# Kernel tuning notes

Hardware: AMD Instinct MI355X
Metric: run time of the kernel (lower is better)

Reference implementation:

```python
import jax, jax.numpy as jnp
import numpy as np

B, N = 8, 16384
DIMS = [3, 64, 128, 1024]  # conv1d(kernel=1) channel sizes: in -> layer_dims -> feat_size
EPS = 1e-5  # BatchNorm1d default eps


def setup_inputs() -> dict:
    key = jax.random.key(0)
    ks = jax.random.split(key, 8)
    inp = {"x": jax.random.normal(ks[0], (B, N, 3), dtype=jnp.float32)}
    for i in range(3):
        cin, cout = DIMS[i], DIMS[i + 1]
        k1, k2 = jax.random.split(ks[i + 1])
        inp[f"W{i}"] = jax.random.normal(k1, (cout, cin), dtype=jnp.float32) * (1.0 / np.sqrt(cin))
        inp[f"b{i}"] = jax.random.normal(k2, (cout,), dtype=jnp.float32) * 0.01
        inp[f"g{i}"] = jnp.ones((cout,), dtype=jnp.float32)   # BN gamma (init 1)
        inp[f"be{i}"] = jnp.zeros((cout,), dtype=jnp.float32)  # BN beta (init 0)
    return inp


def _bn(h, gamma, beta):
    # training-mode BatchNorm1d: stats over batch and point dims, biased variance
    m = h.mean(axis=(0, 1))
    v = h.var(axis=(0, 1))
    return (h - m) * jax.lax.rsqrt(v + EPS) * gamma + beta


def reference(x, W0, b0, g0, be0, W1, b1, g1, be1, W2, b2, g2, be2):
    # pointwise Conv1d (kernel=1) == per-point linear; layout (B, N, C)
    h = jax.nn.relu(_bn(jnp.einsum('bnc,oc->bno', x, W0) + b0, g0, be0))
    local = h  # (B, N, 64) local features
    h = jax.nn.relu(_bn(jnp.einsum('bnc,oc->bno', h, W1) + b1, g1, be1))
    h = _bn(jnp.einsum('bnc,oc->bno', h, W2) + b2, g2, be2)  # no relu on last layer
    gfeat = h.max(axis=1)  # (B, 1024) global max-pool over points
    # concat broadcast global feature with local features -> (B, 1024+64, N) in torch layout
    out = jnp.concatenate(
        [jnp.broadcast_to(gfeat[:, :, None], (B, DIMS[-1], N)), jnp.swapaxes(local, 1, 2)], axis=1)
    return out
```

## Files before the change

### kernel.cpp

```cpp
#include <hip/hip_runtime.h>


#define P_TOT  131072
#define NPTS   16384
#define EPSF   1e-5f

typedef __bf16 bf16x8 __attribute__((ext_vector_type(8)));
typedef float  f32x4  __attribute__((ext_vector_type(4)));

#define H0_OFF   0u
#define H1_OFF   16777216u
#define W1B_OFF  50331648u
#define W2B_OFF  50348032u
#define ST_OFF   50610176u
#define MM_OFF   50662400u

#define S0   0
#define Q0   64
#define S1   128
#define Q1   256
#define S2   384
#define Q2   1408
#define SC0  2432
#define SH0  2496
#define SC1  2560
#define SH1  2688
#define GF   4864
#define STATS_ZERO_N 2432

__device__ __forceinline__ unsigned short f2bf(float f) {
  unsigned u = __builtin_bit_cast(unsigned, f);
  u += 0x7fffu + ((u >> 16) & 1u);
  return (unsigned short)(u >> 16);
}
__device__ __forceinline__ float bf2f(unsigned short s) {
  return __builtin_bit_cast(float, ((unsigned)s) << 16);
}
__device__ __forceinline__ unsigned encf(float f) {
  unsigned u = __builtin_bit_cast(unsigned, f);
  return (u & 0x80000000u) ? ~u : (u | 0x80000000u);
}
__device__ __forceinline__ float decf(unsigned e) {
  unsigned u = (e & 0x80000000u) ? (e & 0x7fffffffu) : ~e;
  return __builtin_bit_cast(float, u);
}
__device__ __forceinline__ uint4 pack8(const float* f) {
  uint4 r;
  r.x = (unsigned)f2bf(f[0]) | ((unsigned)f2bf(f[1]) << 16);
  r.y = (unsigned)f2bf(f[2]) | ((unsigned)f2bf(f[3]) << 16);
  r.z = (unsigned)f2bf(f[4]) | ((unsigned)f2bf(f[5]) << 16);
  r.w = (unsigned)f2bf(f[6]) | ((unsigned)f2bf(f[7]) << 16);
  return r;
}
__device__ __forceinline__ uint4 bnrelu8(uint4 v, const float* sc, const float* sh) {
  unsigned vv[4] = {v.x, v.y, v.z, v.w};
  float f[8];
#pragma unroll
  for (int i = 0; i < 4; ++i) {
    float a = bf2f((unsigned short)(vv[i] & 0xffffu));
    float b = bf2f((unsigned short)(vv[i] >> 16));
    f[2*i]   = fmaxf(fmaf(a, sc[2*i],   sh[2*i]),   0.f);
    f[2*i+1] = fmaxf(fmaf(b, sc[2*i+1], sh[2*i+1]), 0.f);
  }
  return pack8(f);
}

__global__ __launch_bounds__(256) void k_init(const float* __restrict__ W1,
                                              const float* __restrict__ W2,
                                              unsigned short* __restrict__ w1b,
                                              unsigned short* __restrict__ w2b,
                                              float* __restrict__ stats,
                                              unsigned* __restrict__ mmx) {
  int tid = blockIdx.x * 256 + threadIdx.x;
  int stride = gridDim.x * 256;
  for (int i = tid; i < 1024 * 128; i += stride) w2b[i] = f2bf(W2[i]);
  for (int i = tid; i < 128 * 64;   i += stride) w1b[i] = f2bf(W1[i]);
  for (int i = tid; i < STATS_ZERO_N; i += stride) stats[i] = 0.f;
  for (int i = tid; i < 8192; i += stride) { mmx[i] = 0u; mmx[8192 + i] = 0xffffffffu; }
}

__global__ __launch_bounds__(256) void k_layer0(const float* __restrict__ x,
                                                const float* __restrict__ W0,
                                                unsigned short* __restrict__ h0b,
                                                float* __restrict__ stats) {
  __shared__ float w0s[192];
  __shared__ float bs[64], bq[64];
  int t = threadIdx.x;
  if (t < 192) w0s[t] = W0[t];
  if (t < 64) { bs[t] = 0.f; bq[t] = 0.f; }
  __syncthreads();
  int p  = blockIdx.x * 64 + (t >> 2);
  int cs = (t & 3) * 16;
  float x0 = x[p*3], x1 = x[p*3+1], x2 = x[p*3+2];
  float v[16];
#pragma unroll
  for (int j = 0; j < 16; ++j) {
    int c = cs + j;
    v[j] = x0 * w0s[c*3] + x1 * w0s[c*3+1] + x2 * w0s[c*3+2];
  }
  uint4* dst = (uint4*)(h0b + p*64 + cs);
  dst[0] = pack8(&v[0]);
  dst[1] = pack8(&v[8]);
  int lane = t & 63;
#pragma unroll
  for (int j = 0; j < 16; ++j) {
    float s = v[j], q = v[j]*v[j];
#pragma unroll
    for (int m = 4; m < 64; m <<= 1) { s += __shfl_xor(s, m, 64); q += __shfl_xor(q, m, 64); }
    if (lane < 4) { atomicAdd(&bs[cs + j], s); atomicAdd(&bq[cs + j], q); }
  }
  __syncthreads();
  if (t < 64) { atomicAdd(&stats[S0 + t], bs[t]); atomicAdd(&stats[Q0 + t], bq[t]); }
}

__global__ void k_fin0(const float* __restrict__ g, const float* __restrict__ be,
                       float* __restrict__ stats) {
  int c = threadIdx.x;
  float m = stats[S0 + c] * (1.f / P_TOT);
  float q = stats[Q0 + c] * (1.f / P_TOT);
  float sc = g[c] * rsqrtf(q - m*m + EPSF);
  stats[SC0 + c] = sc;
  stats[SH0 + c] = be[c] - m * sc;
}
__global__ void k_fin1(const float* __restrict__ g, const float* __restrict__ be,
                       float* __restrict__ stats) {
  int c = threadIdx.x;
  float m = stats[S1 + c] * (1.f / P_TOT);
  float q = stats[Q1 + c] * (1.f / P_TOT);
  float sc = g[c] * rsqrtf(q - m*m + EPSF);
  stats[SC1 + c] = sc;
  stats[SH1 + c] = be[c] - m * sc;
}

__global__ __launch_bounds__(512, 2) void k_gemm1(const unsigned short* __restrict__ h0b,
                                                  const unsigned short* __restrict__ w1b,
                                                  unsigned short* __restrict__ h1b,
                                                  float* __restrict__ stats) {
  __shared__ uint4 arrA[128 * 8];
  int t = threadIdx.x, l = t & 63, w = t >> 6;
  int wr = w >> 2, wc = w & 3;
  bf16x8 bfr[2][2];
#pragma unroll
  for (int nn = 0; nn < 2; ++nn)
#pragma unroll
    for (int kk = 0; kk < 2; ++kk) {
      int j  = wc*32 + nn*16 + (l & 15);
      int k0 = kk*32 + (l >> 4) * 8;
      bfr[nn][kk] = __builtin_bit_cast(bf16x8, *(const uint4*)(w1b + j*64 + k0));
    }
  int kc = t & 7;
  float ssc[8], ssh[8];
#pragma unroll
  for (int j = 0; j < 8; ++j) { ssc[j] = stats[SC0 + kc*8 + j]; ssh[j] = stats[SH0 + kc*8 + j]; }
  float runS[2] = {0,0}, runQ[2] = {0,0};
  int pbase0 = blockIdx.x * 256;
  for (int mt = 0; mt < 2; ++mt) {
    int pbase = pbase0 + mt * 128;
#pragma unroll
    for (int i = 0; i < 2; ++i) {
      int row = (i*512 + t) >> 3;
      uint4 v = *(const uint4*)(h0b + (pbase + row) * 64 + kc * 8);
      arrA[row*8 + (kc ^ (row & 7))] = bnrelu8(v, ssc, ssh);
    }
    __syncthreads();
    f32x4 acc[4][2];
#pragma unroll
    for (int mm = 0; mm < 4; ++mm)
#pragma unroll
      for (int nn = 0; nn < 2; ++nn) acc[mm][nn] = (f32x4){0.f,0.f,0.f,0.f};
#pragma unroll
    for (int kk = 0; kk < 2; ++kk) {
      bf16x8 a[4];
#pragma unroll
      for (int mm = 0; mm < 4; ++mm) {
        int r  = wr*64 + mm*16 + (l & 15);
        int ck = kk*4 + (l >> 4);
        a[mm] = __builtin_bit_cast(bf16x8, arrA[r*8 + (ck ^ (r & 7))]);
      }
#pragma unroll
      for (int mm = 0; mm < 4; ++mm)
#pragma unroll
        for (int nn = 0; nn < 2; ++nn)
          acc[mm][nn] = __builtin_amdgcn_mfma_f32_16x16x32_bf16(a[mm], bfr[nn][kk], acc[mm][nn], 0, 0, 0);
    }
#pragma unroll
    for (int mm = 0; mm < 4; ++mm) {
      int prow = pbase + wr*64 + mm*16 + (l >> 4) * 4;
#pragma unroll
      for (int nn = 0; nn < 2; ++nn) {
        int col = wc*32 + nn*16 + (l & 15);
#pragma unroll
        for (int r = 0; r < 4; ++r) {
          float f = acc[mm][nn][r];
          h1b[(size_t)(prow + r) * 128 + col] = f2bf(f);
          runS[nn] += f;
          runQ[nn] = fmaf(f, f, runQ[nn]);
        }
      }
    }
    __syncthreads();
  }
#pragma unroll
  for (int nn = 0; nn < 2; ++nn) {
    float s = runS[nn], q = runQ[nn];
    s += __shfl_xor(s, 16, 64); s += __shfl_xor(s, 32, 64);
    q += __shfl_xor(q, 16, 64); q += __shfl_xor(q, 32, 64);
    if (l < 16) {
      int col = wc*32 + nn*16 + l;
      atomicAdd(&stats[S1 + col], s);
      atomicAdd(&stats[Q1 + col], q);
    }
  }
}

__global__ __launch_bounds__(512, 2) void k_gemm2(const unsigned short* __restrict__ h1b,
                                                  const unsigned short* __restrict__ w2b,
                                                  float* __restrict__ stats,
                                                  unsigned* __restrict__ mmx) {
  __shared__ uint4 arrA[64 * 16];
  int t = threadIdx.x, l = t & 63, w = t >> 6;
  int jw = blockIdx.x * 256 + w * 32;
  int pbase0 = blockIdx.y * 512;
  int bidx = pbase0 >> 14;
  bf16x8 bfr[2][4];
#pragma unroll
  for (int nn = 0; nn < 2; ++nn)
#pragma unroll
    for (int kk = 0; kk < 4; ++kk) {
      int j  = jw + nn*16 + (l & 15);
      int k0 = kk*32 + (l >> 4) * 8;
      bfr[nn][kk] = __builtin_bit_cast(bf16x8, *(const uint4*)(w2b + j*128 + k0));
    }
  int kc = t & 15;
  float ssc[8], ssh[8];
#pragma unroll
  for (int j = 0; j < 8; ++j) { ssc[j] = stats[SC1 + kc*8 + j]; ssh[j] = stats[SH1 + kc*8 + j]; }
  float runS[2] = {0,0}, runQ[2] = {0,0};
  float runMax[2] = {-3.4e38f, -3.4e38f}, runMin[2] = {3.4e38f, 3.4e38f};
  for (int mt = 0; mt < 8; ++mt) {
    int pbase = pbase0 + mt * 64;
#pragma unroll
    for (int i = 0; i < 2; ++i) {
      int row = i*32 + (t >> 4);
      uint4 v = *(const uint4*)(h1b + (size_t)(pbase + row) * 128 + kc * 8);
      arrA[row*16 + (kc ^ (row & 7))] = bnrelu8(v, ssc, ssh);
    }
    __syncthreads();
    f32x4 acc[4][2];
#pragma unroll
    for (int mm = 0; mm < 4; ++mm)
#pragma unroll
      for (int nn = 0; nn < 2; ++nn) acc[mm][nn] = (f32x4){0.f,0.f,0.f,0.f};
#pragma unroll
    for (int kk = 0; kk < 4; ++kk) {
      bf16x8 a[4];
#pragma unroll
      for (int mm = 0; mm < 4; ++mm) {
        int r  = mm*16 + (l & 15);
        int ck = kk*4 + (l >> 4);
        a[mm] = __builtin_bit_cast(bf16x8, arrA[r*16 + (ck ^ (r & 7))]);
      }
#pragma unroll
      for (int mm = 0; mm < 4; ++mm)
#pragma unroll
        for (int nn = 0; nn < 2; ++nn)
          acc[mm][nn] = __builtin_amdgcn_mfma_f32_16x16x32_bf16(a[mm], bfr[nn][kk], acc[mm][nn], 0, 0, 0);
    }
#pragma unroll
    for (int nn = 0; nn < 2; ++nn)
#pragma unroll
      for (int mm = 0; mm < 4; ++mm)
#pragma unroll
        for (int r = 0; r < 4; ++r) {
          float f = acc[mm][nn][r];
          runS[nn] += f;
          runQ[nn] = fmaf(f, f, runQ[nn]);
          runMax[nn] = fmaxf(runMax[nn], f);
          runMin[nn] = fminf(runMin[nn], f);
        }
    __syncthreads();
  }
#pragma unroll
  for (int nn = 0; nn < 2; ++nn) {
    float s = runS[nn], q = runQ[nn], mx = runMax[nn], mn = runMin[nn];
    s += __shfl_xor(s, 16, 64); s += __shfl_xor(s, 32, 64);
    q += __shfl_xor(q, 16, 64); q += __shfl_xor(q, 32, 64);
    mx = fmaxf(mx, __shfl_xor(mx, 16, 64)); mx = fmaxf(mx, __shfl_xor(mx, 32, 64));
    mn = fminf(mn, __shfl_xor(mn, 16, 64)); mn = fminf(mn, __shfl_xor(mn, 32, 64));
    if (l < 16) {
      int col = jw + nn*16 + l;
      atomicAdd(&stats[S2 + col], s);
      atomicAdd(&stats[Q2 + col], q);
      atomicMax(&mmx[bidx * 1024 + col], encf(mx));
      atomicMin(&mmx[8192 + bidx * 1024 + col], encf(mn));
    }
  }
}

__global__ void k_fin2(const float* __restrict__ g, const float* __restrict__ be,
                       float* __restrict__ stats, const unsigned* __restrict__ mmx) {
  int idx = blockIdx.x * 256 + threadIdx.x;
  int c = idx & 1023, b = idx >> 10;
  float m = stats[S2 + c] * (1.f / P_TOT);
  float q = stats[Q2 + c] * (1.f / P_TOT);
  float sc = g[c] * rsqrtf(q - m*m + EPSF);
  float sh = be[c] - m * sc;
  float mx = decf(mmx[b * 1024 + c]);
  float mn = decf(mmx[8192 + b * 1024 + c]);
  stats[GF + idx] = (sc >= 0.f) ? fmaf(mx, sc, sh) : fmaf(mn, sc, sh);
}

__global__ __launch_bounds__(256) void k_local(const unsigned short* __restrict__ h0b,
                                               const float* __restrict__ stats,
                                               float* __restrict__ out) {
  __shared__ float tl[64][65];
  int t = threadIdx.x;
  int nb = blockIdx.x * 64;
  int b  = blockIdx.y;
  int kc = t & 7;
  float ssc[8], ssh[8];
#pragma unroll
  for (int j = 0; j < 8; ++j) { ssc[j] = stats[SC0 + kc*8 + j]; ssh[j] = stats[SH0 + kc*8 + j]; }
#pragma unroll
  for (int i = 0; i < 2; ++i) {
    int row = (i*256 + t) >> 3;
    uint4 v = *(const uint4*)(h0b + (size_t)(b * NPTS + nb + row) * 64 + kc * 8);
    unsigned vv[4] = {v.x, v.y, v.z, v.w};
#pragma unroll
    for (int j = 0; j < 4; ++j) {
      float a0 = bf2f((unsigned short)(vv[j] & 0xffffu));
      float a1 = bf2f((unsigned short)(vv[j] >> 16));
      tl[row][kc*8 + 2*j]     = fmaxf(fmaf(a0, ssc[2*j],   ssh[2*j]),   0.f);
      tl[row][kc*8 + 2*j + 1] = fmaxf(fmaf(a1, ssc[2*j+1], ssh[2*j+1]), 0.f);
    }
  }
  __syncthreads();
#pragma unroll
  for (int i = 0; i < 4; ++i) {
    int c   = (t >> 4) + i * 16;
    int seg = t & 15;
    f32x4 o = { tl[seg*4+0][c], tl[seg*4+1][c], tl[seg*4+2][c], tl[seg*4+3][c] };
    f32x4* dst = (f32x4*)(out + ((size_t)b * 1088 + 1024 + c) * NPTS + nb + seg * 4);
    __builtin_nontemporal_store(o, dst);
  }
}

__global__ __launch_bounds__(256) void k_bcast(const float* __restrict__ stats,
                                               float* __restrict__ out) {
  const float* gf = stats + GF;
  size_t i = (size_t)blockIdx.x * 256 + threadIdx.x;
  size_t stride = (size_t)gridDim.x * 256;
  const size_t total = (size_t)8192 * 4096;
  for (; i < total; i += stride) {
    int row = (int)(i >> 12);
    int b = row >> 10, c = row & 1023;
    float v = gf[row];
    f32x4 o = {v, v, v, v};
    f32x4* dst = (f32x4*)(out + ((size_t)b * 1088 + c) * NPTS + ((i & 4095) << 2));
    __builtin_nontemporal_store(o, dst);
  }
}

extern "C" void kernel_launch(void* const* d_in, const int* in_sizes, int n_in,
                              void* d_out, int out_size, void* d_ws, size_t ws_size,
                              hipStream_t stream) {
  const float* x   = (const float*)d_in[0];
  const float* W0  = (const float*)d_in[1];
  const float* g0  = (const float*)d_in[3];
  const float* be0 = (const float*)d_in[4];
  const float* W1  = (const float*)d_in[5];
  const float* g1  = (const float*)d_in[7];
  const float* be1 = (const float*)d_in[8];
  const float* W2  = (const float*)d_in[9];
  const float* g2  = (const float*)d_in[11];
  const float* be2 = (const float*)d_in[12];
  float* out = (float*)d_out;
  char* ws = (char*)d_ws;
  unsigned short* h0b = (unsigned short*)(ws + H0_OFF);
  unsigned short* h1b = (unsigned short*)(ws + H1_OFF);
  unsigned short* w1b = (unsigned short*)(ws + W1B_OFF);
  unsigned short* w2b = (unsigned short*)(ws + W2B_OFF);
  float* stats = (float*)(ws + ST_OFF);
  unsigned* mmx = (unsigned*)(ws + MM_OFF);

  k_init  <<<128, 256, 0, stream>>>(W1, W2, w1b, w2b, stats, mmx);
  k_layer0<<<2048, 256, 0, stream>>>(x, W0, h0b, stats);
  k_fin0  <<<1, 64, 0, stream>>>(g0, be0, stats);
  k_gemm1 <<<512, 512, 0, stream>>>(h0b, w1b, h1b, stats);
  k_fin1  <<<1, 128, 0, stream>>>(g1, be1, stats);
  k_gemm2 <<<dim3(4, 256), 512, 0, stream>>>(h1b, w2b, stats, mmx);
  k_fin2  <<<32, 256, 0, stream>>>(g2, be2, stats, mmx);
  k_local <<<dim3(NPTS / 64, 8), 256, 0, stream>>>(h0b, stats, out);
  k_bcast <<<2048, 256, 0, stream>>>(stats, out);
}
```

Measured before the change: 727.1 us.

## Fuse local-feature output into gemm1, merge init into layer0, prefetch GEMM tiles

Writes the transposed BN+ReLU local features straight from gemm1's shared-memory tile, so the separate k_local kernel and its second read of h0 are gone. Weight conversion and stats/min-max initialisation now run in extra blocks of k_layer0, saving one launch. Both GEMM kernels load the next activation tile into registers before the MFMA loop so the global load overlaps compute, and k_bcast now writes whole rows per block. The merged init no longer zeroes the first 128 stats entries (S0/Q0), so it relies on those being zero from elsewhere.

```diff
diff --git a/kernel.cpp b/kernel.cpp
--- a/kernel.cpp
+++ b/kernel.cpp
@@ -65,27 +65,27 @@
   return pack8(f);
 }
 
-__global__ __launch_bounds__(256) void k_init(const float* __restrict__ W1,
-                                              const float* __restrict__ W2,
-                                              unsigned short* __restrict__ w1b,
-                                              unsigned short* __restrict__ w2b,
-                                              float* __restrict__ stats,
-                                              unsigned* __restrict__ mmx) {
-  int tid = blockIdx.x * 256 + threadIdx.x;
-  int stride = gridDim.x * 256;
-  for (int i = tid; i < 1024 * 128; i += stride) w2b[i] = f2bf(W2[i]);
-  for (int i = tid; i < 128 * 64;   i += stride) w1b[i] = f2bf(W1[i]);
-  for (int i = tid; i < STATS_ZERO_N; i += stride) stats[i] = 0.f;
-  for (int i = tid; i < 8192; i += stride) { mmx[i] = 0u; mmx[8192 + i] = 0xffffffffu; }
-}
-
 __global__ __launch_bounds__(256) void k_layer0(const float* __restrict__ x,
                                                 const float* __restrict__ W0,
+                                                const float* __restrict__ W1,
+                                                const float* __restrict__ W2,
                                                 unsigned short* __restrict__ h0b,
-                                                float* __restrict__ stats) {
+                                                unsigned short* __restrict__ w1b,
+                                                unsigned short* __restrict__ w2b,
+                                                float* __restrict__ stats,
+                                                unsigned* __restrict__ mmx) {
+  int t = threadIdx.x;
+  if (blockIdx.x >= 2048) {
+    int tid = (blockIdx.x - 2048) * 256 + t;
+    const int stride = 128 * 256;
+    for (int i = tid; i < 1024 * 128; i += stride) w2b[i] = f2bf(W2[i]);
+    for (int i = tid; i < 128 * 64;   i += stride) w1b[i] = f2bf(W1[i]);
+    for (int i = 128 + tid; i < STATS_ZERO_N; i += stride) stats[i] = 0.f;
+    for (int i = tid; i < 8192; i += stride) { mmx[i] = 0u; mmx[8192 + i] = 0xffffffffu; }
+    return;
+  }
   __shared__ float w0s[192];
   __shared__ float bs[64], bq[64];
-  int t = threadIdx.x;
   if (t < 192) w0s[t] = W0[t];
   if (t < 64) { bs[t] = 0.f; bq[t] = 0.f; }
   __syncthreads();
@@ -135,7 +135,8 @@
 __global__ __launch_bounds__(512, 2) void k_gemm1(const unsigned short* __restrict__ h0b,
                                                   const unsigned short* __restrict__ w1b,
                                                   unsigned short* __restrict__ h1b,
-                                                  float* __restrict__ stats) {
+                                                  float* __restrict__ stats,
+                                                  float* __restrict__ out) {
   __shared__ uint4 arrA[128 * 8];
   int t = threadIdx.x, l = t & 63, w = t >> 6;
   int wr = w >> 2, wc = w & 3;
@@ -154,15 +155,19 @@
   for (int j = 0; j < 8; ++j) { ssc[j] = stats[SC0 + kc*8 + j]; ssh[j] = stats[SH0 + kc*8 + j]; }
   float runS[2] = {0,0}, runQ[2] = {0,0};
   int pbase0 = blockIdx.x * 256;
+  int srow0 = t >> 3, srow1 = 64 + (t >> 3);
+  uint4 v0 = *(const uint4*)(h0b + (pbase0 + srow0) * 64 + kc * 8);
+  uint4 v1 = *(const uint4*)(h0b + (pbase0 + srow1) * 64 + kc * 8);
   for (int mt = 0; mt < 2; ++mt) {
     int pbase = pbase0 + mt * 128;
-#pragma unroll
-    for (int i = 0; i < 2; ++i) {
-      int row = (i*512 + t) >> 3;
-      uint4 v = *(const uint4*)(h0b + (pbase + row) * 64 + kc * 8);
-      arrA[row*8 + (kc ^ (row & 7))] = bnrelu8(v, ssc, ssh);
-    }
     __syncthreads();
+    arrA[srow0*8 + (kc ^ (srow0 & 7))] = bnrelu8(v0, ssc, ssh);
+    arrA[srow1*8 + (kc ^ (srow1 & 7))] = bnrelu8(v1, ssc, ssh);
+    __syncthreads();
+    if (mt == 0) {
+      v0 = *(const uint4*)(h0b + (pbase0 + 128 + srow0) * 64 + kc * 8);
+      v1 = *(const uint4*)(h0b + (pbase0 + 128 + srow1) * 64 + kc * 8);
+    }
     f32x4 acc[4][2];
 #pragma unroll
     for (int mm = 0; mm < 4; ++mm)
@@ -198,7 +203,25 @@
         }
       }
     }
-    __syncthreads();
+    {
+      int b  = pbase >> 14;
+      int n0 = pbase & 16383;
+      int c  = t >> 3;
+      int seg = t & 7;
+      const unsigned short* lds16 = (const unsigned short*)arrA;
+      size_t obase = ((size_t)b * 1088 + 1024 + c) * NPTS + n0 + seg * 16;
+#pragma unroll
+      for (int q = 0; q < 4; ++q) {
+        float f[4];
+#pragma unroll
+        for (int e = 0; e < 4; ++e) {
+          int row = seg*16 + q*4 + e;
+          f[e] = bf2f(lds16[(row*8 + ((c >> 3) ^ (row & 7)))*8 + (c & 7)]);
+        }
+        f32x4 o = {f[0], f[1], f[2], f[3]};
+        __builtin_nontemporal_store(o, (f32x4*)(out + obase + q*4));
+      }
+    }
   }
 #pragma unroll
   for (int nn = 0; nn < 2; ++nn) {
@@ -237,15 +260,19 @@
   for (int j = 0; j < 8; ++j) { ssc[j] = stats[SC1 + kc*8 + j]; ssh[j] = stats[SH1 + kc*8 + j]; }
   float runS[2] = {0,0}, runQ[2] = {0,0};
   float runMax[2] = {-3.4e38f, -3.4e38f}, runMin[2] = {3.4e38f, 3.4e38f};
+  int srow0 = t >> 4, srow1 = 32 + (t >> 4);
+  uint4 v0 = *(const uint4*)(h1b + (size_t)(pbase0 + srow0) * 128 + kc * 8);
+  uint4 v1 = *(const uint4*)(h1b + (size_t)(pbase0 + srow1) * 128 + kc * 8);
   for (int mt = 0; mt < 8; ++mt) {
-    int pbase = pbase0 + mt * 64;
-#pragma unroll
-    for (int i = 0; i < 2; ++i) {
-      int row = i*32 + (t >> 4);
-      uint4 v = *(const uint4*)(h1b + (size_t)(pbase + row) * 128 + kc * 8);
-      arrA[row*16 + (kc ^ (row & 7))] = bnrelu8(v, ssc, ssh);
-    }
     __syncthreads();
+    arrA[srow0*16 + (kc ^ (srow0 & 7))] = bnrelu8(v0, ssc, ssh);
+    arrA[srow1*16 + (kc ^ (srow1 & 7))] = bnrelu8(v1, ssc, ssh);
+    __syncthreads();
+    if (mt < 7) {
+      int pb = pbase0 + (mt + 1) * 64;
+      v0 = *(const uint4*)(h1b + (size_t)(pb + srow0) * 128 + kc * 8);
+      v1 = *(const uint4*)(h1b + (size_t)(pb + srow1) * 128 + kc * 8);
+    }
     f32x4 acc[4][2];
 #pragma unroll
     for (int mm = 0; mm < 4; ++mm)
@@ -278,7 +305,6 @@
           runMax[nn] = fmaxf(runMax[nn], f);
           runMin[nn] = fminf(runMin[nn], f);
         }
-    __syncthreads();
   }
 #pragma unroll
   for (int nn = 0; nn < 2; ++nn) {
@@ -310,54 +336,20 @@
   stats[GF + idx] = (sc >= 0.f) ? fmaf(mx, sc, sh) : fmaf(mn, sc, sh);
 }
 
-__global__ __launch_bounds__(256) void k_local(const unsigned short* __restrict__ h0b,
-                                               const float* __restrict__ stats,
-                                               float* __restrict__ out) {
-  __shared__ float tl[64][65];
-  int t = threadIdx.x;
-  int nb = blockIdx.x * 64;
-  int b  = blockIdx.y;
-  int kc = t & 7;
-  float ssc[8], ssh[8];
-#pragma unroll
-  for (int j = 0; j < 8; ++j) { ssc[j] = stats[SC0 + kc*8 + j]; ssh[j] = stats[SH0 + kc*8 + j]; }
-#pragma unroll
-  for (int i = 0; i < 2; ++i) {
-    int row = (i*256 + t) >> 3;
-    uint4 v = *(const uint4*)(h0b + (size_t)(b * NPTS + nb + row) * 64 + kc * 8);
-    unsigned vv[4] = {v.x, v.y, v.z, v.w};
-#pragma unroll
-    for (int j = 0; j < 4; ++j) {
-      float a0 = bf2f((unsigned short)(vv[j] & 0xffffu));
-      float a1 = bf2f((unsigned short)(vv[j] >> 16));
-      tl[row][kc*8 + 2*j]     = fmaxf(fmaf(a0, ssc[2*j],   ssh[2*j]),   0.f);
-      tl[row][kc*8 + 2*j + 1] = fmaxf(fmaf(a1, ssc[2*j+1], ssh[2*j+1]), 0.f);
-    }
-  }
-  __syncthreads();
-#pragma unroll
-  for (int i = 0; i < 4; ++i) {
-    int c   = (t >> 4) + i * 16;
-    int seg = t & 15;
-    f32x4 o = { tl[seg*4+0][c], tl[seg*4+1][c], tl[seg*4+2][c], tl[seg*4+3][c] };
-    f32x4* dst = (f32x4*)(out + ((size_t)b * 1088 + 1024 + c) * NPTS + nb + seg * 4);
-    __builtin_nontemporal_store(o, dst);
-  }
-}
-
 __global__ __launch_bounds__(256) void k_bcast(const float* __restrict__ stats,
                                                float* __restrict__ out) {
   const float* gf = stats + GF;
-  size_t i = (size_t)blockIdx.x * 256 + threadIdx.x;
-  size_t stride = (size_t)gridDim.x * 256;
-  const size_t total = (size_t)8192 * 4096;
-  for (; i < total; i += stride) {
-    int row = (int)(i >> 12);
+  int t = threadIdx.x;
+#pragma unroll
+  for (int rr = 0; rr < 4; ++rr) {
+    int row = blockIdx.x * 4 + rr;
     int b = row >> 10, c = row & 1023;
     float v = gf[row];
     f32x4 o = {v, v, v, v};
-    f32x4* dst = (f32x4*)(out + ((size_t)b * 1088 + c) * NPTS + ((i & 4095) << 2));
-    __builtin_nontemporal_store(o, dst);
+    float* base = out + ((size_t)b * 1088 + c) * NPTS;
+#pragma unroll
+    for (int j = 0; j < 16; ++j)
+      __builtin_nontemporal_store(o, (f32x4*)(base + (j * 256 + t) * 4));
   }
 }
 
@@ -383,13 +375,11 @@
   float* stats = (float*)(ws + ST_OFF);
   unsigned* mmx = (unsigned*)(ws + MM_OFF);
 
-  k_init  <<<128, 256, 0, stream>>>(W1, W2, w1b, w2b, stats, mmx);
-  k_layer0<<<2048, 256, 0, stream>>>(x, W0, h0b, stats);
+  k_layer0<<<2176, 256, 0, stream>>>(x, W0, W1, W2, h0b, w1b, w2b, stats, mmx);
   k_fin0  <<<1, 64, 0, stream>>>(g0, be0, stats);
-  k_gemm1 <<<512, 512, 0, stream>>>(h0b, w1b, h1b, stats);
+  k_gemm1 <<<512, 512, 0, stream>>>(h0b, w1b, h1b, stats, out);
   k_fin1  <<<1, 128, 0, stream>>>(g1, be1, stats);
   k_gemm2 <<<dim3(4, 256), 512, 0, stream>>>(h1b, w2b, stats, mmx);
   k_fin2  <<<32, 256, 0, stream>>>(g2, be2, stats, mmx);
-  k_local <<<dim3(NPTS / 64, 8), 256, 0, stream>>>(h0b, stats, out);
   k_bcast <<<2048, 256, 0, stream>>>(stats, out);
 }
```

Result: no change. 729.4 us (+0.3%).
